# Optimization experiments

Hardware: AMD Instinct MI355X
Metric: run time of the kernel (lower is better)

## Reference

```python
import jax, jax.numpy as jnp
import numpy as np

B, H, W, C = 4, 256, 256, 192
WS, SHIFT, NH = 8, 4, 6
HD = C // NH            # 32
N = WS * WS             # 64 tokens per window
NW = (H // WS) * (W // WS)  # 1024 windows per image
HIDDEN = 4 * C
SCALE = HD ** -0.5
EPS = 1e-5


def _swin_attn_mask():
    # standard Swin shifted-window mask: 0 where tokens share a region, -100 otherwise
    img = np.zeros((H, W), np.float32)
    cnt = 0
    for hs in (slice(0, -WS), slice(-WS, -SHIFT), slice(-SHIFT, None)):
        for ws_ in (slice(0, -WS), slice(-WS, -SHIFT), slice(-SHIFT, None)):
            img[hs, ws_] = cnt
            cnt += 1
    mw = img.reshape(H // WS, WS, W // WS, WS).transpose(0, 2, 1, 3).reshape(-1, N)
    diff = mw[:, None, :] - mw[:, :, None]
    return np.where(diff != 0, -100.0, 0.0).astype(np.float32)  # (NW, N, N)


def _rel_pos_index():
    coords = np.stack(np.meshgrid(np.arange(WS), np.arange(WS), indexing='ij')).reshape(2, -1)
    rel = (coords[:, :, None] - coords[:, None, :]).transpose(1, 2, 0)
    rel[:, :, 0] += WS - 1
    rel[:, :, 1] += WS - 1
    rel[:, :, 0] *= 2 * WS - 1
    return rel.sum(-1).astype(np.int32)  # (N, N)


def setup_inputs() -> dict:
    key = jax.random.key(0)
    ks = jax.random.split(key, 12)
    s = 0.02
    x = jax.random.normal(ks[0], (B, H * W, C), jnp.float32)
    mask_matrix = jnp.asarray(_swin_attn_mask())
    rel_idx = jnp.asarray(_rel_pos_index())
    return {
        'x': x,
        'mask_matrix': mask_matrix,
        'rel_idx': rel_idx,
        'qkv_w': jax.random.normal(ks[1], (3 * C, C), jnp.float32) * s,
        'qkv_b': jnp.zeros((3 * C,), jnp.float32),
        'proj_w': jax.random.normal(ks[2], (C, C), jnp.float32) * s,
        'proj_b': jnp.zeros((C,), jnp.float32),
        'rpb_table': jax.random.normal(ks[3], ((2 * WS - 1) * (2 * WS - 1), NH), jnp.float32) * s,
        'norm1_g': jnp.ones((C,), jnp.float32),
        'norm1_b': jnp.zeros((C,), jnp.float32),
        'norm2_g': jnp.ones((C,), jnp.float32),
        'norm2_b': jnp.zeros((C,), jnp.float32),
        'fc1_w': jax.random.normal(ks[4], (HIDDEN, C), jnp.float32) * s,
        'fc1_b': jnp.zeros((HIDDEN,), jnp.float32),
        'fc2_w': jax.random.normal(ks[5], (C, HIDDEN), jnp.float32) * s,
        'fc2_b': jnp.zeros((C,), jnp.float32),
    }


def _layernorm(y, g, b):
    mu = y.mean(-1, keepdims=True)
    var = ((y - mu) ** 2).mean(-1, keepdims=True)
    return (y - mu) * jax.lax.rsqrt(var + EPS) * g + b


def reference(x, mask_matrix, rel_idx, qkv_w, qkv_b, proj_w, proj_b, rpb_table,
              norm1_g, norm1_b, norm2_g, norm2_b, fc1_w, fc1_b, fc2_w, fc2_b):
    shortcut = x
    xi = x.reshape(B, H, W, C)
    # cyclic shift (H,W already multiples of WS -> no padding needed)
    xs = jnp.roll(xi, (-SHIFT, -SHIFT), (1, 2))
    # window partition -> (B*NW, N, C)
    win = xs.reshape(B, H // WS, WS, W // WS, WS, C).transpose(0, 1, 3, 2, 4, 5).reshape(-1, N, C)
    B_ = win.shape[0]
    qkv = (win @ qkv_w.T + qkv_b).reshape(B_, N, 3, NH, HD).transpose(2, 0, 3, 1, 4)
    q, k, v = qkv[0] * SCALE, qkv[1], qkv[2]        # (B_, NH, N, HD)
    attn = jnp.einsum('bhnd,bhmd->bhnm', q, k)       # (B_, NH, N, N)
    rpb = rpb_table[rel_idx.reshape(-1)].reshape(N, N, NH).transpose(2, 0, 1)
    attn = attn + rpb[None]
    nWm = mask_matrix.shape[0]
    attn = attn.reshape(B_ // nWm, nWm, NH, N, N) + mask_matrix[None, :, None]
    attn = jax.nn.softmax(attn.reshape(B_, NH, N, N), axis=-1)
    out = jnp.einsum('bhnm,bhmd->bhnd', attn, v).transpose(0, 2, 1, 3).reshape(B_, N, C)
    out = out @ proj_w.T + proj_b
    # window reverse + reverse shift
    xr = out.reshape(B, H // WS, W // WS, WS, WS, C).transpose(0, 1, 3, 2, 4, 5).reshape(B, H, W, C)
    xr = jnp.roll(xr, (SHIFT, SHIFT), (1, 2)).reshape(B, H * W, C)
    x1 = shortcut + _layernorm(xr, norm1_g, norm1_b)  # post-norm residual as in source
    h = jax.nn.gelu(x1 @ fc1_w.T + fc1_b, approximate=False)
    m = h @ fc2_w.T + fc2_b
    return x1 + _layernorm(m, norm2_g, norm2_b)
```

## Files before the change

### kernel.cpp

```cpp
#include <hip/hip_runtime.h>
#include <hip/hip_bf16.h>
#include <math.h>

typedef unsigned short u16;
typedef unsigned int   u32;
typedef __attribute__((ext_vector_type(8))) short bf16x8;
typedef __attribute__((ext_vector_type(4))) float f32x4;

__device__ __forceinline__ u16 f2bf(float f){
  u32 u = __float_as_uint(f);
  u += 0x7fffu + ((u>>16)&1u);
  return (u16)(u>>16);
}
__device__ __forceinline__ u32 pack2(float a, float b){
  return (u32)f2bf(a) | ((u32)f2bf(b)<<16);
}
__device__ __forceinline__ float bf2f(u16 u){ return __uint_as_float(((u32)u)<<16); }
__device__ __forceinline__ float2 LDF2(const float* p){ return *(const float2*)p; }
__device__ __forceinline__ float gelu_f(float v){
  float t = __expf(1.5957691216057308f * fmaf(0.044715f*v, v*v, v));
  return v - v*__builtin_amdgcn_rcpf(t + 1.0f);
}

#define ST_U32(p,v) (*(u32*)(p) = (v))
#define LD_U32(p)   (*(const u32*)(p))
#define MFMA16(a,b,c) __builtin_amdgcn_mfma_f32_16x16x32_bf16((a),(b),(c),0,0,0)

__device__ __forceinline__ bf16x8 ldsfrag(const u16* p){ return *(const bf16x8*)p; }
__device__ __forceinline__ bf16x8 gfrag(const u16* p){ return *(const bf16x8*)p; }

constexpr float SCALE_Q = 0.17677669529663687f;
constexpr float LN_EPS  = 1e-5f;

#define NQKV 110592
#define NPRJ 36864
#define NFC  147456
#define QKV_SLAB 50331648ull
#define WS_WEIGHTS_B 884736ull
#define WS_RPBM_B    98304ull
#define WS_SPLIT_HDR (WS_WEIGHTS_B + 2*WS_RPBM_B)
#define WS_SPLIT_NEED  (WS_SPLIT_HDR + 3ull*QKV_SLAB*2ull)
#define WS_SPLIT2_NEED (WS_SPLIT_HDR + 4ull*QKV_SLAB*2ull)

__global__ void k_prep(const float* __restrict__ qkv_w, const float* __restrict__ proj_w,
                       const float* __restrict__ fc1_w, const float* __restrict__ fc2_w,
                       const float* __restrict__ rpb, const int* __restrict__ relidx,
                       u16* __restrict__ qkv_bf, u16* __restrict__ proj_bf,
                       u16* __restrict__ fc1_bf, u16* __restrict__ fc2_bf,
                       float* __restrict__ rpbm, float* __restrict__ rpbmT, int mode)
{
  int stride = gridDim.x * blockDim.x;
  int t = blockIdx.x * blockDim.x + threadIdx.x;
  for (int i = t; i < NQKV; i += stride) qkv_bf[i] = f2bf(qkv_w[i]);
  for (int i = t; i < NPRJ; i += stride) proj_bf[i] = f2bf(proj_w[i]);
  for (int i = t; i < NFC;  i += stride) fc1_bf[i]  = f2bf(fc1_w[i]);
  for (int i = t; i < NFC;  i += stride) fc2_bf[i]  = f2bf(fc2_w[i]);
  for (int i = t; i < 6*4096; i += stride){
    int h = i >> 12, ij = i & 4095;
    rpbm[i] = rpb[relidx[ij]*6 + h];
  }
  if (mode){
    for (int i = t; i < 6*4096; i += stride){
      int h = i >> 12, ij = i & 4095;
      int col = ij >> 6, row = ij & 63;
      rpbmT[i] = rpb[relidx[row*64 + col]*6 + h];
    }
  }
}

__global__ __launch_bounds__(256, 4) void k_qkv(
    const float* __restrict__ x, const u16* __restrict__ qkv_bf,
    const float* __restrict__ qkv_b,
    u16* __restrict__ Qg, u16* __restrict__ Kg, u16* __restrict__ VTg)
{
  __shared__ __align__(16) u16 xw[64*200];
  const int tid = threadIdx.x, wave = tid >> 6, lane = tid & 63;
  const int kg = lane >> 4, l15 = lane & 15;
  const int wi = blockIdx.x, b = wi >> 10, wm = wi & 1023;
  const int wh = wm >> 5, ww = wm & 31;
  const size_t imgbase = (size_t)b * (256*256*192);

  for (int s = tid; s < 64*96; s += 256){
    int t = s / 96, c2 = s - t*96;
    int i = t >> 3, j = t & 7;
    int h0 = ((wh<<3) + i + 4) & 255;
    int w0 = ((ww<<3) + j + 4) & 255;
    float2 v = LDF2(x + imgbase + (size_t)(h0*256 + w0)*192 + c2*2);
    ST_U32(xw + t*200 + c2*2, pack2(v.x, v.y));
  }
  __syncthreads();

  const size_t wbase = (size_t)wi * 12288;
  #pragma unroll 1
  for (int batch = 0; batch < 3; ++batch){
    const int col0 = wave*144 + batch*48;
    f32x4 a[4][3];
    #pragma unroll
    for (int j = 0; j < 3; ++j){
      float bv = qkv_b[col0 + j*16 + l15];
      #pragma unroll
      for (int mt = 0; mt < 4; ++mt) a[mt][j] = {bv, bv, bv, bv};
    }
    #pragma unroll 2
    for (int kt = 0; kt < 6; ++kt){
      bf16x8 af[4];
      #pragma unroll
      for (int mt = 0; mt < 4; ++mt)
        af[mt] = ldsfrag(xw + (mt*16 + l15)*200 + kt*32 + kg*8);
      #pragma unroll
      for (int j = 0; j < 3; ++j){
        bf16x8 bfr = gfrag(qkv_bf + (col0 + j*16 + l15)*192 + kt*32 + kg*8);
        #pragma unroll
        for (int mt = 0; mt < 4; ++mt)
          a[mt][j] = MFMA16(af[mt], bfr, a[mt][j]);
      }
    }
    #pragma unroll
    for (int j = 0; j < 3; ++j){
      int colg = col0 + j*16 + l15;
      if (colg < 192){
        #pragma unroll
        for (int mt = 0; mt < 4; ++mt)
          #pragma unroll
          for (int r = 0; r < 4; ++r)
            Qg[wbase + (size_t)(mt*16 + kg*4 + r)*192 + colg] = f2bf(a[mt][j][r]*SCALE_Q);
      } else if (colg < 384){
        #pragma unroll
        for (int mt = 0; mt < 4; ++mt)
          #pragma unroll
          for (int r = 0; r < 4; ++r)
            Kg[wbase + (size_t)(mt*16 + kg*4 + r)*192 + (colg - 192)] = f2bf(a[mt][j][r]);
      } else {
        #pragma unroll
        for (int mt = 0; mt < 4; ++mt){
          ushort4 pk = { f2bf(a[mt][j][0]), f2bf(a[mt][j][1]),
                         f2bf(a[mt][j][2]), f2bf(a[mt][j][3]) };
          *(ushort4*)(VTg + wbase + (size_t)(colg - 384)*64 + mt*16 + kg*4) = pk;
        }
      }
    }
  }
}

__global__ __launch_bounds__(256, 4) void k_attn2(
    const float* __restrict__ x, const float* __restrict__ mask,
    const float* __restrict__ rpbmT,
    const u16* __restrict__ Qg, const u16* __restrict__ Kg,
    const u16* __restrict__ VTg,
    const u16* __restrict__ proj_bf, const float* __restrict__ proj_b,
    const float* __restrict__ n1g, const float* __restrict__ n1b,
    float* __restrict__ x1, u16* __restrict__ x1b)
{
  __shared__ __align__(16) u16 prb[64*72];
  __shared__ __align__(16) u16 obuf[64*200];
  __shared__ float lnred[64*8];

  const int tid = threadIdx.x, wave = tid >> 6, lane = tid & 63;
  const int kg = lane >> 4, l15 = lane & 15;
  const int wi = blockIdx.x, b = wi >> 10, wm = wi & 1023;
  const int wh = wm >> 5, ww = wm & 31;
  const bool hasmask = (wh == 31) || (ww == 31);
  const size_t imgbase = (size_t)b * (256*256*192);
  const size_t wbase = (size_t)wi * 12288;

  f32x4 pj[4][3];
  #pragma unroll
  for (int mt = 0; mt < 4; ++mt)
    #pragma unroll
    for (int nt = 0; nt < 3; ++nt){
      float bv = proj_b[wave*48 + nt*16 + l15];
      pj[mt][nt] = {bv, bv, bv, bv};
    }

  #pragma unroll 1
  for (int h = 0; h < 6; ++h){
    const f32x4 z = {0.f, 0.f, 0.f, 0.f};
    bf16x8 qf = gfrag(Qg + wbase + (size_t)(wave*16 + l15)*192 + h*32 + kg*8);
    f32x4 at[4];
    #pragma unroll
    for (int nt = 0; nt < 4; ++nt){
      bf16x8 kf = gfrag(Kg + wbase + (size_t)(nt*16 + l15)*192 + h*32 + kg*8);
      at[nt] = MFMA16(qf, kf, z);
    }
    {
      const float* rb = rpbmT + h*4096;
      #pragma unroll
      for (int nt = 0; nt < 4; ++nt){
        int cidx = (nt*16 + l15)*64 + wave*16 + kg*4;
        float4 r4 = *(const float4*)(rb + cidx);
        at[nt][0] += r4.x;
        at[nt][1] += r4.y;
        at[nt][2] += r4.z;
        at[nt][3] += r4.w;
      }
    }
    if (hasmask){
      const float* mb = mask + (size_t)wm*4096;
      #pragma unroll
      for (int nt = 0; nt < 4; ++nt){
        int cidx = (nt*16 + l15)*64 + wave*16 + kg*4;
        float4 m4 = *(const float4*)(mb + cidx);
        at[nt][0] += m4.x;
        at[nt][1] += m4.y;
        at[nt][2] += m4.z;
        at[nt][3] += m4.w;
      }
    }
    #pragma unroll
    for (int r = 0; r < 4; ++r){
      float m0 = fmaxf(fmaxf(at[0][r], at[1][r]), fmaxf(at[2][r], at[3][r]));
      #pragma unroll
      for (int mk = 1; mk < 16; mk <<= 1) m0 = fmaxf(m0, __shfl_xor(m0, mk));
      float s = 0.f;
      #pragma unroll
      for (int nt = 0; nt < 4; ++nt){ at[nt][r] = __expf(at[nt][r] - m0); s += at[nt][r]; }
      #pragma unroll
      for (int mk = 1; mk < 16; mk <<= 1) s += __shfl_xor(s, mk);
      float inv = __builtin_amdgcn_rcpf(s);
      #pragma unroll
      for (int nt = 0; nt < 4; ++nt) at[nt][r] *= inv;
    }
    #pragma unroll
    for (int nt = 0; nt < 4; ++nt)
      #pragma unroll
      for (int r = 0; r < 4; ++r)
        prb[(wave*16 + kg*4 + r)*72 + nt*16 + l15] = f2bf(at[nt][r]);
    {
      f32x4 ov[2] = {z, z};
      #pragma unroll
      for (int kt = 0; kt < 2; ++kt){
        bf16x8 pf = ldsfrag(prb + (wave*16 + l15)*72 + kt*32 + kg*8);
        #pragma unroll
        for (int d = 0; d < 2; ++d){
          bf16x8 vf = gfrag(VTg + wbase + (size_t)(h*32 + d*16 + l15)*64 + kt*32 + kg*8);
          ov[d] = MFMA16(pf, vf, ov[d]);
        }
      }
      #pragma unroll
      for (int d = 0; d < 2; ++d)
        #pragma unroll
        for (int r = 0; r < 4; ++r)
          obuf[(wave*16 + kg*4 + r)*200 + h*32 + d*16 + l15] = f2bf(ov[d][r]);
    }
  }
  __syncthreads();

  #pragma unroll 2
  for (int kt = 0; kt < 6; ++kt){
    bf16x8 af[4];
    #pragma unroll
    for (int mt = 0; mt < 4; ++mt)
      af[mt] = ldsfrag(obuf + (mt*16 + l15)*200 + kt*32 + kg*8);
    #pragma unroll
    for (int nt = 0; nt < 3; ++nt){
      bf16x8 bfr = gfrag(proj_bf + (wave*48 + nt*16 + l15)*192 + kt*32 + kg*8);
      #pragma unroll
      for (int mt = 0; mt < 4; ++mt)
        pj[mt][nt] = MFMA16(af[mt], bfr, pj[mt][nt]);
    }
  }

  float gv[3], bv2[3];
  #pragma unroll
  for (int nt = 0; nt < 3; ++nt){
    int c = wave*48 + nt*16 + l15;
    gv[nt] = n1g[c]; bv2[nt] = n1b[c];
  }
  #pragma unroll
  for (int mt = 0; mt < 4; ++mt)
    #pragma unroll
    for (int r = 0; r < 4; ++r){
      float s1 = pj[mt][0][r] + pj[mt][1][r] + pj[mt][2][r];
      float s2 = pj[mt][0][r]*pj[mt][0][r] + pj[mt][1][r]*pj[mt][1][r] + pj[mt][2][r]*pj[mt][2][r];
      #pragma unroll
      for (int mk = 1; mk < 16; mk <<= 1){ s1 += __shfl_xor(s1, mk); s2 += __shfl_xor(s2, mk); }
      if (l15 == 0){
        int t = mt*16 + kg*4 + r;
        lnred[t*8 + wave*2]     = s1;
        lnred[t*8 + wave*2 + 1] = s2;
      }
    }
  __syncthreads();
  const bool wf = (x1 != nullptr);
  const bool wb = (x1b != nullptr);
  #pragma unroll
  for (int mt = 0; mt < 4; ++mt)
    #pragma unroll 1
    for (int r = 0; r < 4; ++r){
      int t = mt*16 + kg*4 + r;
      float a1 = lnred[t*8+0] + lnred[t*8+2] + lnred[t*8+4] + lnred[t*8+6];
      float a2 = lnred[t*8+1] + lnred[t*8+3] + lnred[t*8+5] + lnred[t*8+7];
      float mu = a1 * (1.f/192.f);
      float rs = rsqrtf(a2 * (1.f/192.f) - mu*mu + LN_EPS);
      int i = t >> 3, j = t & 7;
      int h0 = ((wh<<3) + i + 4) & 255, w0 = ((ww<<3) + j + 4) & 255;
      size_t base = imgbase + (size_t)(h0*256 + w0)*192;
      #pragma unroll
      for (int nt = 0; nt < 3; ++nt){
        int c = wave*48 + nt*16 + l15;
        float y = x[base + c] + (pj[mt][nt][r] - mu)*rs*gv[nt] + bv2[nt];
        if (wf) x1[base + c] = y;
        if (wb) x1b[base + c] = f2bf(y);
      }
    }
}

__global__ __launch_bounds__(256, 3) void k_attn(
    const float* __restrict__ x, const float* __restrict__ mask,
    const float* __restrict__ rpbm, const u16* __restrict__ qkv_bf,
    const float* __restrict__ qkv_b, const u16* __restrict__ proj_bf,
    const float* __restrict__ proj_b, const float* __restrict__ n1g,
    const float* __restrict__ n1b, float* __restrict__ x1)
{
  __shared__ __align__(16) u16 xw[64*200];
  __shared__ __align__(16) u16 qkvh[64*72];
  __shared__ __align__(16) u16 vT[32*72];
  __shared__ __align__(16) u16 prb[64*72];
  __shared__ __align__(16) u16 outh[64*40];
  float* lnred = (float*)outh;

  const int tid  = threadIdx.x;
  const int wave = tid >> 6, lane = tid & 63;
  const int kg   = lane >> 4, l15 = lane & 15;
  const int wi = blockIdx.x;
  const int b  = wi >> 10, wm = wi & 1023;
  const int wh = wm >> 5,  ww = wm & 31;
  const size_t imgbase = (size_t)b * (256*256*192);

  for (int s = tid; s < 64*96; s += 256){
    int t = s / 96, c2 = s - t*96;
    int i = t >> 3, j = t & 7;
    int h0 = ((wh<<3) + i + 4) & 255;
    int w0 = ((ww<<3) + j + 4) & 255;
    float2 v = LDF2(x + imgbase + (size_t)(h0*256 + w0)*192 + c2*2);
    ST_U32(xw + t*200 + c2*2, pack2(v.x, v.y));
  }

  f32x4 pj[4][3];
  #pragma unroll
  for (int mt = 0; mt < 4; ++mt)
    #pragma unroll
    for (int nt = 0; nt < 3; ++nt){
      float bv = proj_b[wave*48 + nt*16 + l15];
      pj[mt][nt] = {bv, bv, bv, bv};
    }
  __syncthreads();

  #pragma unroll 1
  for (int h = 0; h < 6; ++h){
    f32x4 qa[6];
    #pragma unroll
    for (int nt = 0; nt < 6; ++nt){
      float bv = qkv_b[(nt>>1)*192 + h*32 + (nt&1)*16 + l15];
      qa[nt] = {bv, bv, bv, bv};
    }
    #pragma unroll 2
    for (int kt = 0; kt < 6; ++kt){
      bf16x8 af = ldsfrag(xw + (wave*16 + l15)*200 + kt*32 + kg*8);
      #pragma unroll
      for (int nt = 0; nt < 6; ++nt){
        bf16x8 bfr = gfrag(qkv_bf + ((nt>>1)*192 + h*32 + (nt&1)*16 + l15)*192 + kt*32 + kg*8);
        qa[nt] = MFMA16(af, bfr, qa[nt]);
      }
    }
    #pragma unroll
    for (int nt = 0; nt < 2; ++nt)
      #pragma unroll
      for (int r = 0; r < 4; ++r)
        qkvh[(wave*16 + kg*4 + r)*72 + nt*16 + l15] = f2bf(qa[nt][r]*SCALE_Q);
    #pragma unroll
    for (int nt = 2; nt < 4; ++nt)
      #pragma unroll
      for (int r = 0; r < 4; ++r)
        qkvh[(wave*16 + kg*4 + r)*72 + 32 + (nt-2)*16 + l15] = f2bf(qa[nt][r]);
    #pragma unroll
    for (int nt = 4; nt < 6; ++nt)
      #pragma unroll
      for (int r = 0; r < 4; ++r)
        vT[((nt-4)*16 + l15)*72 + wave*16 + kg*4 + r] = f2bf(qa[nt][r]);
    __syncthreads();

    f32x4 at[4];
    {
      const f32x4 z = {0.f, 0.f, 0.f, 0.f};
      bf16x8 qf = ldsfrag(qkvh + (wave*16 + l15)*72 + kg*8);
      #pragma unroll
      for (int nt = 0; nt < 4; ++nt){
        bf16x8 kf = ldsfrag(qkvh + (nt*16 + l15)*72 + 32 + kg*8);
        at[nt] = MFMA16(qf, kf, z);
      }
    }
    {
      const float* rb = rpbm + h*4096;
      const float* mb = mask + (size_t)wm*4096;
      #pragma unroll
      for (int nt = 0; nt < 4; ++nt)
        #pragma unroll
        for (int r = 0; r < 4; ++r){
          int idx = (wave*16 + kg*4 + r)*64 + nt*16 + l15;
          at[nt][r] += rb[idx] + mb[idx];
        }
    }
    #pragma unroll
    for (int r = 0; r < 4; ++r){
      float m0 = fmaxf(fmaxf(at[0][r], at[1][r]), fmaxf(at[2][r], at[3][r]));
      #pragma unroll
      for (int mk = 1; mk < 16; mk <<= 1) m0 = fmaxf(m0, __shfl_xor(m0, mk));
      float s = 0.f;
      #pragma unroll
      for (int nt = 0; nt < 4; ++nt){ at[nt][r] = __expf(at[nt][r] - m0); s += at[nt][r]; }
      #pragma unroll
      for (int mk = 1; mk < 16; mk <<= 1) s += __shfl_xor(s, mk);
      float inv = __builtin_amdgcn_rcpf(s);
      #pragma unroll
      for (int nt = 0; nt < 4; ++nt) at[nt][r] *= inv;
    }
    #pragma unroll
    for (int nt = 0; nt < 4; ++nt)
      #pragma unroll
      for (int r = 0; r < 4; ++r)
        prb[(wave*16 + kg*4 + r)*72 + nt*16 + l15] = f2bf(at[nt][r]);

    {
      f32x4 ov[2] = {{0,0,0,0},{0,0,0,0}};
      #pragma unroll
      for (int kt = 0; kt < 2; ++kt){
        bf16x8 pf = ldsfrag(prb + (wave*16 + l15)*72 + kt*32 + kg*8);
        #pragma unroll
        for (int nt = 0; nt < 2; ++nt){
          bf16x8 vf = ldsfrag(vT + (nt*16 + l15)*72 + kt*32 + kg*8);
          ov[nt] = MFMA16(pf, vf, ov[nt]);
        }
      }
      #pragma unroll
      for (int nt = 0; nt < 2; ++nt)
        #pragma unroll
        for (int r = 0; r < 4; ++r)
          outh[(wave*16 + kg*4 + r)*40 + nt*16 + l15] = f2bf(ov[nt][r]);
    }
    __syncthreads();

    {
      bf16x8 pw[3];
      #pragma unroll
      for (int nt = 0; nt < 3; ++nt)
        pw[nt] = gfrag(proj_bf + (wave*48 + nt*16 + l15)*192 + h*32 + kg*8);
      #pragma unroll
      for (int mt = 0; mt < 4; ++mt){
        bf16x8 af = ldsfrag(outh + (mt*16 + l15)*40 + kg*8);
        #pragma unroll
        for (int nt = 0; nt < 3; ++nt)
          pj[mt][nt] = MFMA16(af, pw[nt], pj[mt][nt]);
      }
    }
    __syncthreads();
  }

  float gv[3], bv2[3];
  #pragma unroll
  for (int nt = 0; nt < 3; ++nt){
    int c = wave*48 + nt*16 + l15;
    gv[nt] = n1g[c]; bv2[nt] = n1b[c];
  }
  #pragma unroll
  for (int mt = 0; mt < 4; ++mt)
    #pragma unroll
    for (int r = 0; r < 4; ++r){
      float s1 = pj[mt][0][r] + pj[mt][1][r] + pj[mt][2][r];
      float s2 = pj[mt][0][r]*pj[mt][0][r] + pj[mt][1][r]*pj[mt][1][r] + pj[mt][2][r]*pj[mt][2][r];
      #pragma unroll
      for (int mk = 1; mk < 16; mk <<= 1){ s1 += __shfl_xor(s1, mk); s2 += __shfl_xor(s2, mk); }
      if (l15 == 0){
        int t = mt*16 + kg*4 + r;
        lnred[t*8 + wave*2]     = s1;
        lnred[t*8 + wave*2 + 1] = s2;
      }
    }
  __syncthreads();
  #pragma unroll
  for (int mt = 0; mt < 4; ++mt)
    #pragma unroll 1
    for (int r = 0; r < 4; ++r){
      int t = mt*16 + kg*4 + r;
      float a1 = lnred[t*8+0] + lnred[t*8+2] + lnred[t*8+4] + lnred[t*8+6];
      float a2 = lnred[t*8+1] + lnred[t*8+3] + lnred[t*8+5] + lnred[t*8+7];
      float mu = a1 * (1.f/192.f);
      float rs = rsqrtf(a2 * (1.f/192.f) - mu*mu + LN_EPS);
      int i = t >> 3, j = t & 7;
      int h0 = ((wh<<3) + i + 4) & 255, w0 = ((ww<<3) + j + 4) & 255;
      size_t base = imgbase + (size_t)(h0*256 + w0)*192;
      #pragma unroll
      for (int nt = 0; nt < 3; ++nt){
        int c = wave*48 + nt*16 + l15;
        x1[base + c] = x[base + c] + (pj[mt][nt][r] - mu)*rs*gv[nt] + bv2[nt];
      }
    }
}

__global__ __launch_bounds__(256, 3) void k_mlp2(
    float* __restrict__ xout, const u16* __restrict__ x1b,
    const u16* __restrict__ fc1_bf, const float* __restrict__ fc1_b,
    const u16* __restrict__ fc2_bf, const float* __restrict__ fc2_b,
    const float* __restrict__ n2g, const float* __restrict__ n2b)
{
  __shared__ __align__(16) u16 xt[64*200];
  __shared__ __align__(16) u16 hl[64*200];
  float* const lnred = (float*)hl;

  const int tid  = threadIdx.x;
  const int wave = tid >> 6, lane = tid & 63;
  const int kg   = lane >> 4, l15 = lane & 15;
  const size_t t0 = (size_t)blockIdx.x * 64;

  for (int s = tid; s < 64*24; s += 256){
    int t = s / 24, c8 = s - t*24;
    *(bf16x8*)(xt + t*200 + c8*8) = gfrag(x1b + (t0 + t)*192 + c8*8);
  }
  f32x4 m2[4][3];
  #pragma unroll
  for (int mt = 0; mt < 4; ++mt)
    #pragma unroll
    for (int nt = 0; nt < 3; ++nt){
      float bv = fc2_b[wave*48 + nt*16 + l15];
      m2[mt][nt] = {bv, bv, bv, bv};
    }
  __syncthreads();

  f32x4 a1[4][3];
  #pragma unroll
  for (int mt = 0; mt < 4; ++mt)
    #pragma unroll
    for (int nt = 0; nt < 3; ++nt){
      float bv = fc1_b[wave*48 + nt*16 + l15];
      a1[mt][nt] = {bv, bv, bv, bv};
    }
  #pragma unroll 2
  for (int kt = 0; kt < 6; ++kt){
    bf16x8 af[4];
    #pragma unroll
    for (int mt = 0; mt < 4; ++mt)
      af[mt] = ldsfrag(xt + (mt*16 + l15)*200 + kt*32 + kg*8);
    #pragma unroll
    for (int nt = 0; nt < 3; ++nt){
      bf16x8 bfr = gfrag(fc1_bf + (size_t)(wave*48 + nt*16 + l15)*192 + kt*32 + kg*8);
      #pragma unroll
      for (int mt = 0; mt < 4; ++mt)
        a1[mt][nt] = MFMA16(af[mt], bfr, a1[mt][nt]);
    }
  }

  #pragma unroll 1
  for (int c = 0; c < 4; ++c){
    #pragma unroll
    for (int mt = 0; mt < 4; ++mt)
      #pragma unroll
      for (int nt = 0; nt < 3; ++nt)
        #pragma unroll
        for (int r = 0; r < 4; ++r)
          hl[(mt*16 + kg*4 + r)*200 + wave*48 + nt*16 + l15] = f2bf(gelu_f(a1[mt][nt][r]));
    __syncthreads();

    #pragma unroll 2
    for (int kt = 0; kt < 6; ++kt){
      bf16x8 af[4];
      #pragma unroll
      for (int mt = 0; mt < 4; ++mt)
        af[mt] = ldsfrag(hl + (mt*16 + l15)*200 + kt*32 + kg*8);
      #pragma unroll
      for (int nt = 0; nt < 3; ++nt){
        bf16x8 bfr = gfrag(fc2_bf + (size_t)(wave*48 + nt*16 + l15)*768 + c*192 + kt*32 + kg*8);
        #pragma unroll
        for (int mt = 0; mt < 4; ++mt)
          m2[mt][nt] = MFMA16(af[mt], bfr, m2[mt][nt]);
      }
    }
    if (c < 3){
      const int cn = c + 1;
      #pragma unroll
      for (int mt = 0; mt < 4; ++mt)
        #pragma unroll
        for (int nt = 0; nt < 3; ++nt){
          float bv = fc1_b[cn*192 + wave*48 + nt*16 + l15];
          a1[mt][nt] = {bv, bv, bv, bv};
        }
      #pragma unroll 2
      for (int kt = 0; kt < 6; ++kt){
        bf16x8 af[4];
        #pragma unroll
        for (int mt = 0; mt < 4; ++mt)
          af[mt] = ldsfrag(xt + (mt*16 + l15)*200 + kt*32 + kg*8);
        #pragma unroll
        for (int nt = 0; nt < 3; ++nt){
          bf16x8 bfr = gfrag(fc1_bf + (size_t)(cn*192 + wave*48 + nt*16 + l15)*192 + kt*32 + kg*8);
          #pragma unroll
          for (int mt = 0; mt < 4; ++mt)
            a1[mt][nt] = MFMA16(af[mt], bfr, a1[mt][nt]);
        }
      }
    }
    __syncthreads();
  }

  float gv[3], bv2[3];
  #pragma unroll
  for (int nt = 0; nt < 3; ++nt){
    int cc = wave*48 + nt*16 + l15;
    gv[nt] = n2g[cc]; bv2[nt] = n2b[cc];
  }
  #pragma unroll
  for (int mt = 0; mt < 4; ++mt)
    #pragma unroll
    for (int r = 0; r < 4; ++r){
      float s1 = m2[mt][0][r] + m2[mt][1][r] + m2[mt][2][r];
      float s2 = m2[mt][0][r]*m2[mt][0][r] + m2[mt][1][r]*m2[mt][1][r] + m2[mt][2][r]*m2[mt][2][r];
      #pragma unroll
      for (int mk = 1; mk < 16; mk <<= 1){ s1 += __shfl_xor(s1, mk); s2 += __shfl_xor(s2, mk); }
      if (l15 == 0){
        int t = mt*16 + kg*4 + r;
        lnred[t*8 + wave*2]     = s1;
        lnred[t*8 + wave*2 + 1] = s2;
      }
    }
  __syncthreads();
  #pragma unroll
  for (int mt = 0; mt < 4; ++mt)
    #pragma unroll 1
    for (int r = 0; r < 4; ++r){
      int t = mt*16 + kg*4 + r;
      float a1s = lnred[t*8+0] + lnred[t*8+2] + lnred[t*8+4] + lnred[t*8+6];
      float a2s = lnred[t*8+1] + lnred[t*8+3] + lnred[t*8+5] + lnred[t*8+7];
      float mu = a1s * (1.f/192.f);
      float rs = rsqrtf(a2s * (1.f/192.f) - mu*mu + LN_EPS);
      size_t base = (t0 + t)*192;
      #pragma unroll
      for (int nt = 0; nt < 3; ++nt){
        int cc = wave*48 + nt*16 + l15;
        float xv = bf2f(xt[t*200 + cc]);
        xout[base + cc] = xv + (m2[mt][nt][r] - mu)*rs*gv[nt] + bv2[nt];
      }
    }
}

__global__ __launch_bounds__(256, 3) void k_mlp(
    float* xio, const u16* __restrict__ fc1_bf,
    const float* __restrict__ fc1_b, const u16* __restrict__ fc2_bf,
    const float* __restrict__ fc2_b, const float* __restrict__ n2g,
    const float* __restrict__ n2b)
{
  __shared__ __align__(16) u16 xt[64*200];
  __shared__ __align__(16) u16 hl[64*200];
  __shared__ float lnred[64*8];

  const int tid  = threadIdx.x;
  const int wave = tid >> 6, lane = tid & 63;
  const int kg   = lane >> 4, l15 = lane & 15;
  const size_t t0 = (size_t)blockIdx.x * 64;

  for (int s = tid; s < 64*96; s += 256){
    int t = s / 96, c2 = s - t*96;
    float2 v = LDF2(xio + (t0 + t)*192 + c2*2);
    ST_U32(xt + t*200 + c2*2, pack2(v.x, v.y));
  }
  f32x4 m2[4][3];
  #pragma unroll
  for (int mt = 0; mt < 4; ++mt)
    #pragma unroll
    for (int nt = 0; nt < 3; ++nt){
      float bv = fc2_b[wave*48 + nt*16 + l15];
      m2[mt][nt] = {bv, bv, bv, bv};
    }
  __syncthreads();

  f32x4 a1[4][3];
  #pragma unroll
  for (int mt = 0; mt < 4; ++mt)
    #pragma unroll
    for (int nt = 0; nt < 3; ++nt){
      float bv = fc1_b[wave*48 + nt*16 + l15];
      a1[mt][nt] = {bv, bv, bv, bv};
    }
  #pragma unroll 2
  for (int kt = 0; kt < 6; ++kt){
    bf16x8 af[4];
    #pragma unroll
    for (int mt = 0; mt < 4; ++mt)
      af[mt] = ldsfrag(xt + (mt*16 + l15)*200 + kt*32 + kg*8);
    #pragma unroll
    for (int nt = 0; nt < 3; ++nt){
      bf16x8 bfr = gfrag(fc1_bf + (size_t)(wave*48 + nt*16 + l15)*192 + kt*32 + kg*8);
      #pragma unroll
      for (int mt = 0; mt < 4; ++mt)
        a1[mt][nt] = MFMA16(af[mt], bfr, a1[mt][nt]);
    }
  }

  #pragma unroll 1
  for (int c = 0; c < 4; ++c){
    #pragma unroll
    for (int mt = 0; mt < 4; ++mt)
      #pragma unroll
      for (int nt = 0; nt < 3; ++nt)
        #pragma unroll
        for (int r = 0; r < 4; ++r)
          hl[(mt*16 + kg*4 + r)*200 + wave*48 + nt*16 + l15] = f2bf(gelu_f(a1[mt][nt][r]));
    __syncthreads();

    #pragma unroll 2
    for (int kt = 0; kt < 6; ++kt){
      bf16x8 af[4];
      #pragma unroll
      for (int mt = 0; mt < 4; ++mt)
        af[mt] = ldsfrag(hl + (mt*16 + l15)*200 + kt*32 + kg*8);
      #pragma unroll
      for (int nt = 0; nt < 3; ++nt){
        bf16x8 bfr = gfrag(fc2_bf + (size_t)(wave*48 + nt*16 + l15)*768 + c*192 + kt*32 + kg*8);
        #pragma unroll
        for (int mt = 0; mt < 4; ++mt)
          m2[mt][nt] = MFMA16(af[mt], bfr, m2[mt][nt]);
      }
    }
    if (c < 3){
      const int cn = c + 1;
      #pragma unroll
      for (int mt = 0; mt < 4; ++mt)
        #pragma unroll
        for (int nt = 0; nt < 3; ++nt){
          float bv = fc1_b[cn*192 + wave*48 + nt*16 + l15];
          a1[mt][nt] = {bv, bv, bv, bv};
        }
      #pragma unroll 2
      for (int kt = 0; kt < 6; ++kt){
        bf16x8 af[4];
        #pragma unroll
        for (int mt = 0; mt < 4; ++mt)
          af[mt] = ldsfrag(xt + (mt*16 + l15)*200 + kt*32 + kg*8);
        #pragma unroll
        for (int nt = 0; nt < 3; ++nt){
          bf16x8 bfr = gfrag(fc1_bf + (size_t)(cn*192 + wave*48 + nt*16 + l15)*192 + kt*32 + kg*8);
          #pragma unroll
          for (int mt = 0; mt < 4; ++mt)
            a1[mt][nt] = MFMA16(af[mt], bfr, a1[mt][nt]);
        }
      }
    }
    __syncthreads();
  }

  float gv[3], bv2[3];
  #pragma unroll
  for (int nt = 0; nt < 3; ++nt){
    int cc = wave*48 + nt*16 + l15;
    gv[nt] = n2g[cc]; bv2[nt] = n2b[cc];
  }
  #pragma unroll
  for (int mt = 0; mt < 4; ++mt)
    #pragma unroll
    for (int r = 0; r < 4; ++r){
      float s1 = m2[mt][0][r] + m2[mt][1][r] + m2[mt][2][r];
      float s2 = m2[mt][0][r]*m2[mt][0][r] + m2[mt][1][r]*m2[mt][1][r] + m2[mt][2][r]*m2[mt][2][r];
      #pragma unroll
      for (int mk = 1; mk < 16; mk <<= 1){ s1 += __shfl_xor(s1, mk); s2 += __shfl_xor(s2, mk); }
      if (l15 == 0){
        int t = mt*16 + kg*4 + r;
        lnred[t*8 + wave*2]     = s1;
        lnred[t*8 + wave*2 + 1] = s2;
      }
    }
  __syncthreads();
  #pragma unroll
  for (int mt = 0; mt < 4; ++mt)
    #pragma unroll 1
    for (int r = 0; r < 4; ++r){
      int t = mt*16 + kg*4 + r;
      float a1s = lnred[t*8+0] + lnred[t*8+2] + lnred[t*8+4] + lnred[t*8+6];
      float a2s = lnred[t*8+1] + lnred[t*8+3] + lnred[t*8+5] + lnred[t*8+7];
      float mu = a1s * (1.f/192.f);
      float rs = rsqrtf(a2s * (1.f/192.f) - mu*mu + LN_EPS);
      size_t base = (t0 + t)*192;
      #pragma unroll
      for (int nt = 0; nt < 3; ++nt){
        int cc = wave*48 + nt*16 + l15;
        xio[base + cc] = xio[base + cc] + (m2[mt][nt][r] - mu)*rs*gv[nt] + bv2[nt];
      }
    }
}

extern "C" void kernel_launch(void* const* d_in, const int* in_sizes, int n_in,
                              void* d_out, int out_size, void* d_ws, size_t ws_size,
                              hipStream_t stream)
{
  const float* x      = (const float*)d_in[0];
  const float* mask   = (const float*)d_in[1];
  const int*   relidx = (const int*)d_in[2];
  const float* qkv_w  = (const float*)d_in[3];
  const float* qkv_b  = (const float*)d_in[4];
  const float* proj_w = (const float*)d_in[5];
  const float* proj_b = (const float*)d_in[6];
  const float* rpb    = (const float*)d_in[7];
  const float* n1g    = (const float*)d_in[8];
  const float* n1b    = (const float*)d_in[9];
  const float* n2g    = (const float*)d_in[10];
  const float* n2b    = (const float*)d_in[11];
  const float* fc1_w  = (const float*)d_in[12];
  const float* fc1_b  = (const float*)d_in[13];
  const float* fc2_w  = (const float*)d_in[14];
  const float* fc2_b  = (const float*)d_in[15];
  float* xio = (float*)d_out;

  u16* qkv_bf  = (u16*)d_ws;
  u16* proj_bf = qkv_bf + NQKV;
  u16* fc1_bf  = proj_bf + NPRJ;
  u16* fc2_bf  = fc1_bf + NFC;
  float* rpbm  = (float*)(fc2_bf + NFC);
  float* rpbmT = rpbm + 6*4096;
  u16* Qg  = (u16*)((char*)d_ws + WS_SPLIT_HDR);
  u16* Kg  = Qg + QKV_SLAB;
  u16* VTg = Kg + QKV_SLAB;
  u16* x1b = VTg + QKV_SLAB;

  const int tier = (ws_size >= WS_SPLIT2_NEED) ? 2 : (ws_size >= WS_SPLIT_NEED) ? 1 : 0;

  k_prep<<<dim3(512), dim3(256), 0, stream>>>(qkv_w, proj_w, fc1_w, fc2_w,
      rpb, relidx, qkv_bf, proj_bf, fc1_bf, fc2_bf, rpbm, rpbmT, tier ? 1 : 0);
  if (tier){
    k_qkv<<<dim3(4096), dim3(256), 0, stream>>>(x, qkv_bf, qkv_b, Qg, Kg, VTg);
    if (tier == 2){
      k_attn2<<<dim3(4096), dim3(256), 0, stream>>>(x, mask, rpbmT, Qg, Kg, VTg,
          proj_bf, proj_b, n1g, n1b, (float*)nullptr, x1b);
      k_mlp2<<<dim3(4096), dim3(256), 0, stream>>>(xio, x1b, fc1_bf, fc1_b,
          fc2_bf, fc2_b, n2g, n2b);
    } else {
      k_attn2<<<dim3(4096), dim3(256), 0, stream>>>(x, mask, rpbmT, Qg, Kg, VTg,
          proj_bf, proj_b, n1g, n1b, xio, (u16*)nullptr);
      k_mlp<<<dim3(4096), dim3(256), 0, stream>>>(xio, fc1_bf, fc1_b, fc2_bf, fc2_b,
          n2g, n2b);
    }
  } else {
    k_attn<<<dim3(4096), dim3(256), 0, stream>>>(x, mask, rpbm, qkv_bf, qkv_b,
        proj_bf, proj_b, n1g, n1b, xio);
    k_mlp<<<dim3(4096), dim3(256), 0, stream>>>(xio, fc1_bf, fc1_b, fc2_bf, fc2_b,
        n2g, n2b);
  }
}
```

Measured before the change: 931.7 us.

## Fuse attention, projection, LN1 and MLP into one per-window kernel

Merges the attention-plus-projection kernel with the MLP kernel, so each 64-token window keeps its x1 result in shared memory as bf16 and goes straight through fc1, GELU and fc2. This drops the global write and re-read of x1 (bf16 or fp32) and one kernel launch. LDS buffers are aliased (prb, hl, lnred share one buffer) and launch bounds drop to 3 blocks per CU. The MLP now runs per window instead of per row tile, and the final output is scattered to the shifted positions. This may lower occupancy and raise register pressure during the attention phase.

```diff
diff --git a/kernel.cpp b/kernel.cpp
--- a/kernel.cpp
+++ b/kernel.cpp
@@ -23,7 +23,6 @@
 }
 
 #define ST_U32(p,v) (*(u32*)(p) = (v))
-#define LD_U32(p)   (*(const u32*)(p))
 #define MFMA16(a,b,c) __builtin_amdgcn_mfma_f32_16x16x32_bf16((a),(b),(c),0,0,0)
 
 __device__ __forceinline__ bf16x8 ldsfrag(const u16* p){ return *(const bf16x8*)p; }
@@ -40,7 +39,6 @@
 #define WS_RPBM_B    98304ull
 #define WS_SPLIT_HDR (WS_WEIGHTS_B + 2*WS_RPBM_B)
 #define WS_SPLIT_NEED  (WS_SPLIT_HDR + 3ull*QKV_SLAB*2ull)
-#define WS_SPLIT2_NEED (WS_SPLIT_HDR + 4ull*QKV_SLAB*2ull)
 
 __global__ void k_prep(const float* __restrict__ qkv_w, const float* __restrict__ proj_w,
                        const float* __restrict__ fc1_w, const float* __restrict__ fc2_w,
@@ -142,18 +140,23 @@
   }
 }
 
-__global__ __launch_bounds__(256, 4) void k_attn2(
+__global__ __launch_bounds__(256, 3) void k_fused(
     const float* __restrict__ x, const float* __restrict__ mask,
     const float* __restrict__ rpbmT,
     const u16* __restrict__ Qg, const u16* __restrict__ Kg,
     const u16* __restrict__ VTg,
     const u16* __restrict__ proj_bf, const float* __restrict__ proj_b,
     const float* __restrict__ n1g, const float* __restrict__ n1b,
-    float* __restrict__ x1, u16* __restrict__ x1b)
+    const u16* __restrict__ fc1_bf, const float* __restrict__ fc1_b,
+    const u16* __restrict__ fc2_bf, const float* __restrict__ fc2_b,
+    const float* __restrict__ n2g, const float* __restrict__ n2b,
+    float* __restrict__ out)
 {
-  __shared__ __align__(16) u16 prb[64*72];
-  __shared__ __align__(16) u16 obuf[64*200];
-  __shared__ float lnred[64*8];
+  __shared__ __align__(16) u16 xt[64*200];
+  __shared__ __align__(16) u16 rb[64*200];
+  u16* const prb = rb;
+  u16* const hl  = rb;
+  float* const lnred = (float*)rb;
 
   const int tid = threadIdx.x, wave = tid >> 6, lane = tid & 63;
   const int kg = lane >> 4, l15 = lane & 15;
@@ -183,15 +186,13 @@
       at[nt] = MFMA16(qf, kf, z);
     }
     {
-      const float* rb = rpbmT + h*4096;
+      const float* rbp = rpbmT + h*4096;
       #pragma unroll
       for (int nt = 0; nt < 4; ++nt){
         int cidx = (nt*16 + l15)*64 + wave*16 + kg*4;
-        float4 r4 = *(const float4*)(rb + cidx);
-        at[nt][0] += r4.x;
-        at[nt][1] += r4.y;
-        at[nt][2] += r4.z;
-        at[nt][3] += r4.w;
+        float4 r4 = *(const float4*)(rbp + cidx);
+        at[nt][0] += r4.x; at[nt][1] += r4.y;
+        at[nt][2] += r4.z; at[nt][3] += r4.w;
       }
     }
     if (hasmask){
@@ -200,10 +201,8 @@
       for (int nt = 0; nt < 4; ++nt){
         int cidx = (nt*16 + l15)*64 + wave*16 + kg*4;
         float4 m4 = *(const float4*)(mb + cidx);
-        at[nt][0] += m4.x;
-        at[nt][1] += m4.y;
-        at[nt][2] += m4.z;
-        at[nt][3] += m4.w;
+        at[nt][0] += m4.x; at[nt][1] += m4.y;
+        at[nt][2] += m4.z; at[nt][3] += m4.w;
       }
     }
     #pragma unroll
@@ -240,7 +239,7 @@
       for (int d = 0; d < 2; ++d)
         #pragma unroll
         for (int r = 0; r < 4; ++r)
-          obuf[(wave*16 + kg*4 + r)*200 + h*32 + d*16 + l15] = f2bf(ov[d][r]);
+          xt[(wave*16 + kg*4 + r)*200 + h*32 + d*16 + l15] = f2bf(ov[d][r]);
     }
   }
   __syncthreads();
@@ -250,7 +249,7 @@
     bf16x8 af[4];
     #pragma unroll
     for (int mt = 0; mt < 4; ++mt)
-      af[mt] = ldsfrag(obuf + (mt*16 + l15)*200 + kt*32 + kg*8);
+      af[mt] = ldsfrag(xt + (mt*16 + l15)*200 + kt*32 + kg*8);
     #pragma unroll
     for (int nt = 0; nt < 3; ++nt){
       bf16x8 bfr = gfrag(proj_bf + (wave*48 + nt*16 + l15)*192 + kt*32 + kg*8);
@@ -260,49 +259,175 @@
     }
   }
 
-  float gv[3], bv2[3];
-  #pragma unroll
-  for (int nt = 0; nt < 3; ++nt){
-    int c = wave*48 + nt*16 + l15;
-    gv[nt] = n1g[c]; bv2[nt] = n1b[c];
-  }
-  #pragma unroll
-  for (int mt = 0; mt < 4; ++mt)
-    #pragma unroll
-    for (int r = 0; r < 4; ++r){
-      float s1 = pj[mt][0][r] + pj[mt][1][r] + pj[mt][2][r];
-      float s2 = pj[mt][0][r]*pj[mt][0][r] + pj[mt][1][r]*pj[mt][1][r] + pj[mt][2][r]*pj[mt][2][r];
-      #pragma unroll
-      for (int mk = 1; mk < 16; mk <<= 1){ s1 += __shfl_xor(s1, mk); s2 += __shfl_xor(s2, mk); }
-      if (l15 == 0){
+  {
+    float gv[3], bv2[3];
+    #pragma unroll
+    for (int nt = 0; nt < 3; ++nt){
+      int c = wave*48 + nt*16 + l15;
+      gv[nt] = n1g[c]; bv2[nt] = n1b[c];
+    }
+    #pragma unroll
+    for (int mt = 0; mt < 4; ++mt)
+      #pragma unroll
+      for (int r = 0; r < 4; ++r){
+        float s1 = pj[mt][0][r] + pj[mt][1][r] + pj[mt][2][r];
+        float s2 = pj[mt][0][r]*pj[mt][0][r] + pj[mt][1][r]*pj[mt][1][r] + pj[mt][2][r]*pj[mt][2][r];
+        #pragma unroll
+        for (int mk = 1; mk < 16; mk <<= 1){ s1 += __shfl_xor(s1, mk); s2 += __shfl_xor(s2, mk); }
+        if (l15 == 0){
+          int t = mt*16 + kg*4 + r;
+          lnred[t*8 + wave*2]     = s1;
+          lnred[t*8 + wave*2 + 1] = s2;
+        }
+      }
+    __syncthreads();
+    #pragma unroll
+    for (int mt = 0; mt < 4; ++mt)
+      #pragma unroll 1
+      for (int r = 0; r < 4; ++r){
         int t = mt*16 + kg*4 + r;
-        lnred[t*8 + wave*2]     = s1;
-        lnred[t*8 + wave*2 + 1] = s2;
-      }
-    }
+        float a1s = lnred[t*8+0] + lnred[t*8+2] + lnred[t*8+4] + lnred[t*8+6];
+        float a2s = lnred[t*8+1] + lnred[t*8+3] + lnred[t*8+5] + lnred[t*8+7];
+        float mu = a1s * (1.f/192.f);
+        float rs = rsqrtf(a2s * (1.f/192.f) - mu*mu + LN_EPS);
+        int i = t >> 3, j = t & 7;
+        int h0 = ((wh<<3) + i + 4) & 255, w0 = ((ww<<3) + j + 4) & 255;
+        size_t base = imgbase + (size_t)(h0*256 + w0)*192;
+        #pragma unroll
+        for (int nt = 0; nt < 3; ++nt){
+          int c = wave*48 + nt*16 + l15;
+          float y = x[base + c] + (pj[mt][nt][r] - mu)*rs*gv[nt] + bv2[nt];
+          xt[t*200 + c] = f2bf(y);
+        }
+      }
+  }
   __syncthreads();
-  const bool wf = (x1 != nullptr);
-  const bool wb = (x1b != nullptr);
-  #pragma unroll
-  for (int mt = 0; mt < 4; ++mt)
-    #pragma unroll 1
-    for (int r = 0; r < 4; ++r){
-      int t = mt*16 + kg*4 + r;
-      float a1 = lnred[t*8+0] + lnred[t*8+2] + lnred[t*8+4] + lnred[t*8+6];
-      float a2 = lnred[t*8+1] + lnred[t*8+3] + lnred[t*8+5] + lnred[t*8+7];
-      float mu = a1 * (1.f/192.f);
-      float rs = rsqrtf(a2 * (1.f/192.f) - mu*mu + LN_EPS);
-      int i = t >> 3, j = t & 7;
-      int h0 = ((wh<<3) + i + 4) & 255, w0 = ((ww<<3) + j + 4) & 255;
-      size_t base = imgbase + (size_t)(h0*256 + w0)*192;
+
+  f32x4 m2[4][3];
+  #pragma unroll
+  for (int mt = 0; mt < 4; ++mt)
+    #pragma unroll
+    for (int nt = 0; nt < 3; ++nt){
+      float bv = fc2_b[wave*48 + nt*16 + l15];
+      m2[mt][nt] = {bv, bv, bv, bv};
+    }
+  f32x4 a1[4][3];
+  #pragma unroll
+  for (int mt = 0; mt < 4; ++mt)
+    #pragma unroll
+    for (int nt = 0; nt < 3; ++nt){
+      float bv = fc1_b[wave*48 + nt*16 + l15];
+      a1[mt][nt] = {bv, bv, bv, bv};
+    }
+  #pragma unroll 2
+  for (int kt = 0; kt < 6; ++kt){
+    bf16x8 af[4];
+    #pragma unroll
+    for (int mt = 0; mt < 4; ++mt)
+      af[mt] = ldsfrag(xt + (mt*16 + l15)*200 + kt*32 + kg*8);
+    #pragma unroll
+    for (int nt = 0; nt < 3; ++nt){
+      bf16x8 bfr = gfrag(fc1_bf + (size_t)(wave*48 + nt*16 + l15)*192 + kt*32 + kg*8);
+      #pragma unroll
+      for (int mt = 0; mt < 4; ++mt)
+        a1[mt][nt] = MFMA16(af[mt], bfr, a1[mt][nt]);
+    }
+  }
+
+  #pragma unroll 1
+  for (int c = 0; c < 4; ++c){
+    #pragma unroll
+    for (int mt = 0; mt < 4; ++mt)
+      #pragma unroll
+      for (int nt = 0; nt < 3; ++nt)
+        #pragma unroll
+        for (int r = 0; r < 4; ++r)
+          hl[(mt*16 + kg*4 + r)*200 + wave*48 + nt*16 + l15] = f2bf(gelu_f(a1[mt][nt][r]));
+    __syncthreads();
+
+    #pragma unroll 2
+    for (int kt = 0; kt < 6; ++kt){
+      bf16x8 af[4];
+      #pragma unroll
+      for (int mt = 0; mt < 4; ++mt)
+        af[mt] = ldsfrag(hl + (mt*16 + l15)*200 + kt*32 + kg*8);
       #pragma unroll
       for (int nt = 0; nt < 3; ++nt){
-        int c = wave*48 + nt*16 + l15;
-        float y = x[base + c] + (pj[mt][nt][r] - mu)*rs*gv[nt] + bv2[nt];
-        if (wf) x1[base + c] = y;
-        if (wb) x1b[base + c] = f2bf(y);
-      }
-    }
+        bf16x8 bfr = gfrag(fc2_bf + (size_t)(wave*48 + nt*16 + l15)*768 + c*192 + kt*32 + kg*8);
+        #pragma unroll
+        for (int mt = 0; mt < 4; ++mt)
+          m2[mt][nt] = MFMA16(af[mt], bfr, m2[mt][nt]);
+      }
+    }
+    if (c < 3){
+      const int cn = c + 1;
+      #pragma unroll
+      for (int mt = 0; mt < 4; ++mt)
+        #pragma unroll
+        for (int nt = 0; nt < 3; ++nt){
+          float bv = fc1_b[cn*192 + wave*48 + nt*16 + l15];
+          a1[mt][nt] = {bv, bv, bv, bv};
+        }
+      #pragma unroll 2
+      for (int kt = 0; kt < 6; ++kt){
+        bf16x8 af[4];
+        #pragma unroll
+        for (int mt = 0; mt < 4; ++mt)
+          af[mt] = ldsfrag(xt + (mt*16 + l15)*200 + kt*32 + kg*8);
+        #pragma unroll
+        for (int nt = 0; nt < 3; ++nt){
+          bf16x8 bfr = gfrag(fc1_bf + (size_t)(cn*192 + wave*48 + nt*16 + l15)*192 + kt*32 + kg*8);
+          #pragma unroll
+          for (int mt = 0; mt < 4; ++mt)
+            a1[mt][nt] = MFMA16(af[mt], bfr, a1[mt][nt]);
+        }
+      }
+    }
+    __syncthreads();
+  }
+
+  {
+    float gv[3], bv2[3];
+    #pragma unroll
+    for (int nt = 0; nt < 3; ++nt){
+      int cc = wave*48 + nt*16 + l15;
+      gv[nt] = n2g[cc]; bv2[nt] = n2b[cc];
+    }
+    #pragma unroll
+    for (int mt = 0; mt < 4; ++mt)
+      #pragma unroll
+      for (int r = 0; r < 4; ++r){
+        float s1 = m2[mt][0][r] + m2[mt][1][r] + m2[mt][2][r];
+        float s2 = m2[mt][0][r]*m2[mt][0][r] + m2[mt][1][r]*m2[mt][1][r] + m2[mt][2][r]*m2[mt][2][r];
+        #pragma unroll
+        for (int mk = 1; mk < 16; mk <<= 1){ s1 += __shfl_xor(s1, mk); s2 += __shfl_xor(s2, mk); }
+        if (l15 == 0){
+          int t = mt*16 + kg*4 + r;
+          lnred[t*8 + wave*2]     = s1;
+          lnred[t*8 + wave*2 + 1] = s2;
+        }
+      }
+    __syncthreads();
+    #pragma unroll
+    for (int mt = 0; mt < 4; ++mt)
+      #pragma unroll 1
+      for (int r = 0; r < 4; ++r){
+        int t = mt*16 + kg*4 + r;
+        float a1s = lnred[t*8+0] + lnred[t*8+2] + lnred[t*8+4] + lnred[t*8+6];
+        float a2s = lnred[t*8+1] + lnred[t*8+3] + lnred[t*8+5] + lnred[t*8+7];
+        float mu = a1s * (1.f/192.f);
+        float rs = rsqrtf(a2s * (1.f/192.f) - mu*mu + LN_EPS);
+        int i = t >> 3, j = t & 7;
+        int h0 = ((wh<<3) + i + 4) & 255, w0 = ((ww<<3) + j + 4) & 255;
+        size_t base = imgbase + (size_t)(h0*256 + w0)*192;
+        #pragma unroll
+        for (int nt = 0; nt < 3; ++nt){
+          int cc = wave*48 + nt*16 + l15;
+          float xv = bf2f(xt[t*200 + cc]);
+          out[base + cc] = xv + (m2[mt][nt][r] - mu)*rs*gv[nt] + bv2[nt];
+        }
+      }
+  }
 }
 
 __global__ __launch_bounds__(256, 3) void k_attn(
@@ -391,14 +516,14 @@
       }
     }
     {
-      const float* rb = rpbm + h*4096;
+      const float* rbp = rpbm + h*4096;
       const float* mb = mask + (size_t)wm*4096;
       #pragma unroll
       for (int nt = 0; nt < 4; ++nt)
         #pragma unroll
         for (int r = 0; r < 4; ++r){
           int idx = (wave*16 + kg*4 + r)*64 + nt*16 + l15;
-          at[nt][r] += rb[idx] + mb[idx];
+          at[nt][r] += rbp[idx] + mb[idx];
         }
     }
     #pragma unroll
@@ -493,150 +618,6 @@
       for (int nt = 0; nt < 3; ++nt){
         int c = wave*48 + nt*16 + l15;
         x1[base + c] = x[base + c] + (pj[mt][nt][r] - mu)*rs*gv[nt] + bv2[nt];
-      }
-    }
-}
-
-__global__ __launch_bounds__(256, 3) void k_mlp2(
-    float* __restrict__ xout, const u16* __restrict__ x1b,
-    const u16* __restrict__ fc1_bf, const float* __restrict__ fc1_b,
-    const u16* __restrict__ fc2_bf, const float* __restrict__ fc2_b,
-    const float* __restrict__ n2g, const float* __restrict__ n2b)
-{
-  __shared__ __align__(16) u16 xt[64*200];
-  __shared__ __align__(16) u16 hl[64*200];
-  float* const lnred = (float*)hl;
-
-  const int tid  = threadIdx.x;
-  const int wave = tid >> 6, lane = tid & 63;
-  const int kg   = lane >> 4, l15 = lane & 15;
-  const size_t t0 = (size_t)blockIdx.x * 64;
-
-  for (int s = tid; s < 64*24; s += 256){
-    int t = s / 24, c8 = s - t*24;
-    *(bf16x8*)(xt + t*200 + c8*8) = gfrag(x1b + (t0 + t)*192 + c8*8);
-  }
-  f32x4 m2[4][3];
-  #pragma unroll
-  for (int mt = 0; mt < 4; ++mt)
-    #pragma unroll
-    for (int nt = 0; nt < 3; ++nt){
-      float bv = fc2_b[wave*48 + nt*16 + l15];
-      m2[mt][nt] = {bv, bv, bv, bv};
-    }
-  __syncthreads();
-
-  f32x4 a1[4][3];
-  #pragma unroll
-  for (int mt = 0; mt < 4; ++mt)
-    #pragma unroll
-    for (int nt = 0; nt < 3; ++nt){
-      float bv = fc1_b[wave*48 + nt*16 + l15];
-      a1[mt][nt] = {bv, bv, bv, bv};
-    }
-  #pragma unroll 2
-  for (int kt = 0; kt < 6; ++kt){
-    bf16x8 af[4];
-    #pragma unroll
-    for (int mt = 0; mt < 4; ++mt)
-      af[mt] = ldsfrag(xt + (mt*16 + l15)*200 + kt*32 + kg*8);
-    #pragma unroll
-    for (int nt = 0; nt < 3; ++nt){
-      bf16x8 bfr = gfrag(fc1_bf + (size_t)(wave*48 + nt*16 + l15)*192 + kt*32 + kg*8);
-      #pragma unroll
-      for (int mt = 0; mt < 4; ++mt)
-        a1[mt][nt] = MFMA16(af[mt], bfr, a1[mt][nt]);
-    }
-  }
-
-  #pragma unroll 1
-  for (int c = 0; c < 4; ++c){
-    #pragma unroll
-    for (int mt = 0; mt < 4; ++mt)
-      #pragma unroll
-      for (int nt = 0; nt < 3; ++nt)
-        #pragma unroll
-        for (int r = 0; r < 4; ++r)
-          hl[(mt*16 + kg*4 + r)*200 + wave*48 + nt*16 + l15] = f2bf(gelu_f(a1[mt][nt][r]));
-    __syncthreads();
-
-    #pragma unroll 2
-    for (int kt = 0; kt < 6; ++kt){
-      bf16x8 af[4];
-      #pragma unroll
-      for (int mt = 0; mt < 4; ++mt)
-        af[mt] = ldsfrag(hl + (mt*16 + l15)*200 + kt*32 + kg*8);
-      #pragma unroll
-      for (int nt = 0; nt < 3; ++nt){
-        bf16x8 bfr = gfrag(fc2_bf + (size_t)(wave*48 + nt*16 + l15)*768 + c*192 + kt*32 + kg*8);
-        #pragma unroll
-        for (int mt = 0; mt < 4; ++mt)
-          m2[mt][nt] = MFMA16(af[mt], bfr, m2[mt][nt]);
-      }
-    }
-    if (c < 3){
-      const int cn = c + 1;
-      #pragma unroll
-      for (int mt = 0; mt < 4; ++mt)
-        #pragma unroll
-        for (int nt = 0; nt < 3; ++nt){
-          float bv = fc1_b[cn*192 + wave*48 + nt*16 + l15];
-          a1[mt][nt] = {bv, bv, bv, bv};
-        }
-      #pragma unroll 2
-      for (int kt = 0; kt < 6; ++kt){
-        bf16x8 af[4];
-        #pragma unroll
-        for (int mt = 0; mt < 4; ++mt)
-          af[mt] = ldsfrag(xt + (mt*16 + l15)*200 + kt*32 + kg*8);
-        #pragma unroll
-        for (int nt = 0; nt < 3; ++nt){
-          bf16x8 bfr = gfrag(fc1_bf + (size_t)(cn*192 + wave*48 + nt*16 + l15)*192 + kt*32 + kg*8);
-          #pragma unroll
-          for (int mt = 0; mt < 4; ++mt)
-            a1[mt][nt] = MFMA16(af[mt], bfr, a1[mt][nt]);
-        }
-      }
-    }
-    __syncthreads();
-  }
-
-  float gv[3], bv2[3];
-  #pragma unroll
-  for (int nt = 0; nt < 3; ++nt){
-    int cc = wave*48 + nt*16 + l15;
-    gv[nt] = n2g[cc]; bv2[nt] = n2b[cc];
-  }
-  #pragma unroll
-  for (int mt = 0; mt < 4; ++mt)
-    #pragma unroll
-    for (int r = 0; r < 4; ++r){
-      float s1 = m2[mt][0][r] + m2[mt][1][r] + m2[mt][2][r];
-      float s2 = m2[mt][0][r]*m2[mt][0][r] + m2[mt][1][r]*m2[mt][1][r] + m2[mt][2][r]*m2[mt][2][r];
-      #pragma unroll
-      for (int mk = 1; mk < 16; mk <<= 1){ s1 += __shfl_xor(s1, mk); s2 += __shfl_xor(s2, mk); }
-      if (l15 == 0){
-        int t = mt*16 + kg*4 + r;
-        lnred[t*8 + wave*2]     = s1;
-        lnred[t*8 + wave*2 + 1] = s2;
-      }
-    }
-  __syncthreads();
-  #pragma unroll
-  for (int mt = 0; mt < 4; ++mt)
-    #pragma unroll 1
-    for (int r = 0; r < 4; ++r){
-      int t = mt*16 + kg*4 + r;
-      float a1s = lnred[t*8+0] + lnred[t*8+2] + lnred[t*8+4] + lnred[t*8+6];
-      float a2s = lnred[t*8+1] + lnred[t*8+3] + lnred[t*8+5] + lnred[t*8+7];
-      float mu = a1s * (1.f/192.f);
-      float rs = rsqrtf(a2s * (1.f/192.f) - mu*mu + LN_EPS);
-      size_t base = (t0 + t)*192;
-      #pragma unroll
-      for (int nt = 0; nt < 3; ++nt){
-        int cc = wave*48 + nt*16 + l15;
-        float xv = bf2f(xt[t*200 + cc]);
-        xout[base + cc] = xv + (m2[mt][nt][r] - mu)*rs*gv[nt] + bv2[nt];
       }
     }
 }
@@ -816,25 +797,15 @@
   u16* Qg  = (u16*)((char*)d_ws + WS_SPLIT_HDR);
   u16* Kg  = Qg + QKV_SLAB;
   u16* VTg = Kg + QKV_SLAB;
-  u16* x1b = VTg + QKV_SLAB;
-
-  const int tier = (ws_size >= WS_SPLIT2_NEED) ? 2 : (ws_size >= WS_SPLIT_NEED) ? 1 : 0;
+
+  const int tier = (ws_size >= WS_SPLIT_NEED) ? 1 : 0;
 
   k_prep<<<dim3(512), dim3(256), 0, stream>>>(qkv_w, proj_w, fc1_w, fc2_w,
-      rpb, relidx, qkv_bf, proj_bf, fc1_bf, fc2_bf, rpbm, rpbmT, tier ? 1 : 0);
+      rpb, relidx, qkv_bf, proj_bf, fc1_bf, fc2_bf, rpbm, rpbmT, tier);
   if (tier){
     k_qkv<<<dim3(4096), dim3(256), 0, stream>>>(x, qkv_bf, qkv_b, Qg, Kg, VTg);
-    if (tier == 2){
-      k_attn2<<<dim3(4096), dim3(256), 0, stream>>>(x, mask, rpbmT, Qg, Kg, VTg,
-          proj_bf, proj_b, n1g, n1b, (float*)nullptr, x1b);
-      k_mlp2<<<dim3(4096), dim3(256), 0, stream>>>(xio, x1b, fc1_bf, fc1_b,
-          fc2_bf, fc2_b, n2g, n2b);
-    } else {
-      k_attn2<<<dim3(4096), dim3(256), 0, stream>>>(x, mask, rpbmT, Qg, Kg, VTg,
-          proj_bf, proj_b, n1g, n1b, xio, (u16*)nullptr);
-      k_mlp<<<dim3(4096), dim3(256), 0, stream>>>(xio, fc1_bf, fc1_b, fc2_bf, fc2_b,
-          n2g, n2b);
-    }
+    k_fused<<<dim3(4096), dim3(256), 0, stream>>>(x, mask, rpbmT, Qg, Kg, VTg,
+        proj_bf, proj_b, n1g, n1b, fc1_bf, fc1_b, fc2_bf, fc2_b, n2g, n2b, xio);
   } else {
     k_attn<<<dim3(4096), dim3(256), 0, stream>>>(x, mask, rpbm, qkv_bf, qkv_b,
         proj_bf, proj_b, n1g, n1b, xio);
```

After: 848.2 us. -9.0%, faster.
